# Performance work log

Measured on AMD Instinct MI355X. Metric: run time of the kernel, lower is better.

## Reference

```python
import jax, jax.numpy as jnp
import numpy as np

K = 1024
H = 16
HID = 4 * K
EPS = 1e-5


def _layernorm(x, g, b):
    mu = jnp.mean(x, axis=-1, keepdims=True)
    var = jnp.var(x, axis=-1, keepdims=True)
    return (x - mu) * jax.lax.rsqrt(var + EPS) * g + b


def _attention(xq, xkv, wq, wk, wv, wo, bo, causal):
    b, t, e = xq.shape
    tc = xkv.shape[1]
    h, s = H, e // H
    scale = e ** (-0.25)  # applied to both q and k, as in the original
    q = (xq @ wq).reshape(b, t, h, s) * scale
    k = (xkv @ wk).reshape(b, tc, h, s) * scale
    v = (xkv @ wv).reshape(b, tc, h, s)
    dot = jnp.einsum('bqhs,bkhs->bhqk', q, k)  # (b,h,t,tc)
    if causal:
        mask = jnp.tril(jnp.ones((t, tc), dtype=bool))
        dot = jnp.where(mask, dot, jnp.finfo(dot.dtype).min)
    att = jax.nn.softmax(dot, axis=-1)
    out = jnp.einsum('bhqk,bkhs->bqhs', att, v).reshape(b, t, e)
    return out @ wo + bo


def setup_inputs() -> dict:
    key = jax.random.key(0)
    ks = jax.random.split(key, 16)
    sd = K ** -0.5
    inp = {
        'x': jax.random.normal(ks[0], (4, 1024, K), jnp.float32),
        'context': jax.random.normal(ks[1], (4, 1024, K), jnp.float32),
        'sa_wq': jax.random.normal(ks[2], (K, K), jnp.float32) * sd,
        'sa_wk': jax.random.normal(ks[3], (K, K), jnp.float32) * sd,
        'sa_wv': jax.random.normal(ks[4], (K, K), jnp.float32) * sd,
        'sa_wo': jax.random.normal(ks[5], (K, K), jnp.float32) * sd,
        'sa_bo': jnp.zeros((K,), jnp.float32),
        'ca_wq': jax.random.normal(ks[6], (K, K), jnp.float32) * sd,
        'ca_wk': jax.random.normal(ks[7], (K, K), jnp.float32) * sd,
        'ca_wv': jax.random.normal(ks[8], (K, K), jnp.float32) * sd,
        'ca_wo': jax.random.normal(ks[9], (K, K), jnp.float32) * sd,
        'ca_bo': jnp.zeros((K,), jnp.float32),
        'n1_g': jnp.ones((K,), jnp.float32), 'n1_b': jnp.zeros((K,), jnp.float32),
        'n2_g': jnp.ones((K,), jnp.float32), 'n2_b': jnp.zeros((K,), jnp.float32),
        'n3_g': jnp.ones((K,), jnp.float32), 'n3_b': jnp.zeros((K,), jnp.float32),
        'ff_w1': jax.random.normal(ks[10], (K, HID), jnp.float32) * sd,
        'ff_b1': jnp.zeros((HID,), jnp.float32),
        'ff_w2': jax.random.normal(ks[11], (HID, K), jnp.float32) * (HID ** -0.5),
        'ff_b2': jnp.zeros((K,), jnp.float32),
    }
    return inp


def reference(x, context, sa_wq, sa_wk, sa_wv, sa_wo, sa_bo,
              ca_wq, ca_wk, ca_wv, ca_wo, ca_bo,
              n1_g, n1_b, n2_g, n2_b, n3_g, n3_b,
              ff_w1, ff_b1, ff_w2, ff_b2):
    # Masked self-attention + residual + LN (dropout is identity in eval mode)
    sa = _attention(x, x, sa_wq, sa_wk, sa_wv, sa_wo, sa_bo, causal=True)
    x = _layernorm(x + sa, n1_g, n1_b)
    # Cross-attention + residual + LN
    ca = _attention(x, context, ca_wq, ca_wk, ca_wv, ca_wo, ca_bo, causal=False)
    x = _layernorm(x + ca, n2_g, n2_b)
    # FFN + residual + LN
    ff = jax.nn.relu(x @ ff_w1 + ff_b1) @ ff_w2 + ff_b2
    x = _layernorm(x + ff, n3_g, n3_b)
    return x
```

## Files before the change

kernel.cpp:

```cpp
#include <hip/hip_runtime.h>

typedef __bf16 bf16x8 __attribute__((ext_vector_type(8)));
typedef __bf16 bf16x4 __attribute__((ext_vector_type(4)));
typedef float floatx4 __attribute__((ext_vector_type(4)));

#define EMB 1024
#define MROWS 4096
#define HIDN 4096
#define PSTRIDE ((size_t)MROWS * EMB)

__device__ __forceinline__ void load_lds16(const __bf16* g, __bf16* l) {
    __builtin_amdgcn_global_load_lds(
        (const __attribute__((address_space(1))) void*)g,
        (__attribute__((address_space(3))) void*)l, 16, 0, 0);
}

struct TJobs { const float* s[16]; __bf16* d[16]; int sld[16]; int dld[16]; };
__global__ void transpose_cast16_kernel(TJobs a) {
    __shared__ float tile[32][33];
    int jz = blockIdx.z;
    const float* in = a.s[jz];
    __bf16* out = a.d[jz];
    int sld = a.sld[jz], dld = a.dld[jz];
    int tx = threadIdx.x, ty = threadIdx.y;
    int c0 = blockIdx.x * 32, r0 = blockIdx.y * 32;
#pragma unroll
    for (int i = 0; i < 32; i += 8)
        tile[ty + i][tx] = in[(size_t)(r0 + ty + i) * sld + c0 + tx];
    __syncthreads();
#pragma unroll
    for (int i = 0; i < 32; i += 8)
        out[(size_t)(c0 + ty + i) * dld + r0 + tx] = (__bf16)tile[tx][ty + i];
}

__global__ void transpose_v_kernel(const __bf16* __restrict__ in,
                                   __bf16* __restrict__ vt, int ld, int Tc) {
    __shared__ __bf16 tile[32][33];
    int tx = threadIdx.x, ty = threadIdx.y;
    int t0 = blockIdx.x * 32, s0 = blockIdx.y * 32;
    int bh = blockIdx.z, b = bh >> 4, h = bh & 15;
#pragma unroll
    for (int i = 0; i < 32; i += 8)
        tile[ty + i][tx] = in[(size_t)(b * Tc + t0 + ty + i) * ld + h * 64 + s0 + tx];
    __syncthreads();
#pragma unroll
    for (int i = 0; i < 32; i += 8)
        vt[((size_t)bh * 64 + s0 + ty + i) * Tc + t0 + tx] = tile[tx][ty + i];
}

__global__ void cast_bf16_kernel(const float* __restrict__ in,
                                 __bf16* __restrict__ out, int n) {
    int i = (blockIdx.x * 256 + threadIdx.x) * 4;
    if (i >= n) return;
    float4 v = *(const float4*)(in + i);
    bf16x4 o;
    o[0] = (__bf16)v.x; o[1] = (__bf16)v.y; o[2] = (__bf16)v.z; o[3] = (__bf16)v.w;
    *(bf16x4*)(out + i) = o;
}

template <int RELU, int REG>
__launch_bounds__(256, 4)
__global__ void gemm_bt(const __bf16* __restrict__ A, const __bf16* __restrict__ A2,
                        int asplit, const __bf16* __restrict__ Bt,
                        __bf16* __restrict__ cb, __bf16* __restrict__ cbalt,
                        const float* __restrict__ bias,
                        int M, int N, int Kd, float scale0, float scale1,
                        int split, int fx, int fy) {
    __shared__ alignas(16) __bf16 smem[2 * 128 * 32];
    __bf16* As = smem;
    __bf16* Bs = smem + 128 * 32;
    int tid  = threadIdx.x;
    int wv   = tid >> 6, lane = tid & 63;

    int L   = blockIdx.x + gridDim.x * (blockIdx.y + gridDim.y * blockIdx.z);
    int xcd = L & 7, j = L >> 3;
    int ff  = fx * fy;
    int zw  = xcd / ff;
    int rr  = xcd % ff;
    int nxf = gridDim.x / fx;
    int bnw = (j % nxf) * fx + (rr % fx);
    int bmw = (j / nxf) * fy + (rr / fx);
    int bn  = bnw * 128, bm = bmw * 128;

    int wm   = (wv & 1) * 64, wn = (wv >> 1) * 64;
    int l16  = lane & 15, g16 = lane >> 4;

    int kc   = Kd / gridDim.z;
    int zoff = zw * kc;

    const __bf16* Ause = (bn >= asplit) ? A2 : A;

    const __bf16* ag0 = Ause + (size_t)(bm + (tid >> 2)) * Kd + zoff + (tid & 3) * 8;
    const __bf16* ag1 = ag0 + (size_t)64 * Kd;
    const __bf16* bg0 = Bt + (size_t)(bn + (tid >> 2)) * Kd + zoff + (tid & 3) * 8;
    const __bf16* bg1 = bg0 + (size_t)64 * Kd;
    __bf16* al0 = &As[tid * 8];
    __bf16* al1 = &As[2048 + tid * 8];
    __bf16* bl0 = &Bs[tid * 8];
    __bf16* bl1 = &Bs[2048 + tid * 8];

    floatx4 acc[4][4] = {};

    if (REG) {
        bf16x8 pa0 = *(const bf16x8*)ag0;
        bf16x8 pa1 = *(const bf16x8*)ag1;
        bf16x8 pb0 = *(const bf16x8*)bg0;
        bf16x8 pb1 = *(const bf16x8*)bg1;
        for (int k0 = 0; k0 < kc; k0 += 32) {
            *(bf16x8*)al0 = pa0;
            *(bf16x8*)al1 = pa1;
            *(bf16x8*)bl0 = pb0;
            *(bf16x8*)bl1 = pb1;
            if (k0 + 32 < kc) {
                ag0 += 32; ag1 += 32; bg0 += 32; bg1 += 32;
                pa0 = *(const bf16x8*)ag0;
                pa1 = *(const bf16x8*)ag1;
                pb0 = *(const bf16x8*)bg0;
                pb1 = *(const bf16x8*)bg1;
            }
            __syncthreads();
            bf16x8 af[4], bfr[4];
#pragma unroll
            for (int i = 0; i < 4; ++i)
                af[i] = *(const bf16x8*)&As[(wm + i * 16 + l16) * 32 + g16 * 8];
#pragma unroll
            for (int jj = 0; jj < 4; ++jj)
                bfr[jj] = *(const bf16x8*)&Bs[(wn + jj * 16 + l16) * 32 + g16 * 8];
#pragma unroll
            for (int i = 0; i < 4; ++i)
#pragma unroll
                for (int jj = 0; jj < 4; ++jj)
                    acc[i][jj] = __builtin_amdgcn_mfma_f32_16x16x32_bf16(af[i], bfr[jj], acc[i][jj], 0, 0, 0);
            __syncthreads();
        }
    } else {
        for (int k0 = 0; k0 < kc; k0 += 32) {
            __syncthreads();
            load_lds16(ag0, al0); load_lds16(ag1, al1);
            load_lds16(bg0, bl0); load_lds16(bg1, bl1);
            ag0 += 32; ag1 += 32; bg0 += 32; bg1 += 32;
            __syncthreads();
            bf16x8 af[4], bfr[4];
#pragma unroll
            for (int i = 0; i < 4; ++i)
                af[i] = *(const bf16x8*)&As[(wm + i * 16 + l16) * 32 + g16 * 8];
#pragma unroll
            for (int jj = 0; jj < 4; ++jj)
                bfr[jj] = *(const bf16x8*)&Bs[(wn + jj * 16 + l16) * 32 + g16 * 8];
#pragma unroll
            for (int i = 0; i < 4; ++i)
#pragma unroll
                for (int jj = 0; jj < 4; ++jj)
                    acc[i][jj] = __builtin_amdgcn_mfma_f32_16x16x32_bf16(af[i], bfr[jj], acc[i][jj], 0, 0, 0);
        }
        __syncthreads();
    }

    __bf16* Cp = (zw == 0) ? cb : cbalt + (size_t)(zw - 1) * M * N;
    const float* bz = (zw == 0) ? bias : nullptr;

    __bf16* eb = smem + wv * 2048;
    int erow = lane >> 2;
    int ecol = (lane & 3) * 16;
#pragma unroll
    for (int i = 0; i < 4; ++i) {
#pragma unroll
        for (int jj = 0; jj < 4; ++jj) {
            int col  = bn + wn + jj * 16 + l16;
            float sc = (col < split) ? scale0 : scale1;
            float bv = bz ? bz[col] : 0.f;
#pragma unroll
            for (int r = 0; r < 4; ++r) {
                float v = acc[i][jj][r] * sc + bv;
                if (RELU) v = fmaxf(v, 0.f);
                eb[(g16 * 4 + r) * 76 + jj * 16 + l16] = (__bf16)v;
            }
        }
        bf16x8 t0 = *(const bf16x8*)&eb[erow * 76 + ecol];
        bf16x8 t1 = *(const bf16x8*)&eb[erow * 76 + ecol + 8];
        size_t gb = (size_t)(bm + wm + i * 16 + erow) * N + bn + wn + ecol;
        *(bf16x8*)&Cp[gb]     = t0;
        *(bf16x8*)&Cp[gb + 8] = t1;
    }
}

__launch_bounds__(256, 3)
__global__ void attn_kernel(const __bf16* __restrict__ qb, const __bf16* __restrict__ kb,
                            const __bf16* __restrict__ vt, int ldq, int ldk,
                            __bf16* __restrict__ out, int causal, int Tc) {
    constexpr int T = 1024;
    __shared__ alignas(16) __bf16 Qs[128 * 72];
    __shared__ alignas(16) __bf16 Ks[64 * 72];
    __shared__ alignas(16) __bf16 Vs[64 * 72];
    __shared__ alignas(16) __bf16 Ps[4][16 * 72];

    int tid = threadIdx.x;
    int wv = tid >> 6, lane = tid & 63;
    int l16 = lane & 15, g16 = lane >> 4;

    int L = blockIdx.x;
    int xcd = L & 7, idx = L >> 3;
    int i3 = idx & 7;
    int qt2 = (idx & 32) ? (7 - i3) : i3;
    int pair = xcd + 8 * (idx >> 3);
    int h = pair & 15, b = pair >> 4;

    int r0 = tid >> 3, s8 = (tid & 7) * 8;
    int r1 = r0 + 32;

#pragma unroll
    for (int p = 0; p < 4; ++p) {
        int row = r0 + p * 32;
        bf16x8 qv = *(const bf16x8*)(qb + (size_t)(b * T + qt2 * 128 + row) * ldq + h * 64 + s8);
        *(bf16x8*)&Qs[row * 72 + s8] = qv;
    }

    floatx4 oacc[2][4] = {};
    float li[2] = {0.f, 0.f};

    int ktend = causal ? (2 * qt2 + 2) : (Tc / 64);

    const __bf16* kbase = kb + (size_t)b * Tc * ldk + h * 64 + s8;
    const __bf16* vbase = vt + (size_t)(b * 16 + h) * 64 * Tc + s8;

    bf16x8 kc0 = *(const bf16x8*)(kbase + (size_t)r0 * ldk);
    bf16x8 kc1 = *(const bf16x8*)(kbase + (size_t)r1 * ldk);
    bf16x8 vc0 = *(const bf16x8*)(vbase + (size_t)r0 * Tc);
    bf16x8 vc1 = *(const bf16x8*)(vbase + (size_t)r1 * Tc);
    bf16x8 kn0, kn1, vn0, vn1;

    for (int kt = 0; kt < ktend; ++kt) {
        __syncthreads();
        *(bf16x8*)&Ks[r0 * 72 + s8] = kc0;
        *(bf16x8*)&Ks[r1 * 72 + s8] = kc1;
        *(bf16x8*)&Vs[r0 * 72 + s8] = vc0;
        *(bf16x8*)&Vs[r1 * 72 + s8] = vc1;
        if (kt + 1 < ktend) {
            const __bf16* kp = kbase + (size_t)(kt + 1) * 64 * ldk;
            const __bf16* vp = vbase + (size_t)(kt + 1) * 64;
            kn0 = *(const bf16x8*)(kp + (size_t)r0 * ldk);
            kn1 = *(const bf16x8*)(kp + (size_t)r1 * ldk);
            vn0 = *(const bf16x8*)(vp + (size_t)r0 * Tc);
            vn1 = *(const bf16x8*)(vp + (size_t)r1 * Tc);
        }
        __syncthreads();

#pragma unroll
        for (int sub = 0; sub < 2; ++sub) {
            if (causal && kt > 2 * qt2 + sub) continue;

            floatx4 sacc[4] = {};
#pragma unroll
            for (int kk = 0; kk < 2; ++kk) {
                bf16x8 bq = *(const bf16x8*)&Qs[(sub * 64 + wv * 16 + l16) * 72 + kk * 32 + g16 * 8];
#pragma unroll
                for (int j = 0; j < 4; ++j) {
                    bf16x8 ak = *(const bf16x8*)&Ks[(j * 16 + l16) * 72 + kk * 32 + g16 * 8];
                    sacc[j] = __builtin_amdgcn_mfma_f32_16x16x32_bf16(ak, bq, sacc[j], 0, 0, 0);
                }
            }
            if (causal && kt == 2 * qt2 + sub) {
                int qloc = wv * 16 + l16;
#pragma unroll
                for (int j = 0; j < 4; ++j)
#pragma unroll
                    for (int r = 0; r < 4; ++r)
                        if (j * 16 + g16 * 4 + r > qloc) sacc[j][r] = -1e30f;
            }

#pragma unroll
            for (int j = 0; j < 4; ++j) {
                bf16x4 pk;
#pragma unroll
                for (int r = 0; r < 4; ++r) {
                    float p = __builtin_amdgcn_exp2f(sacc[j][r]);
                    li[sub] += p;
                    pk[r] = (__bf16)p;
                }
                *(bf16x4*)&Ps[wv][l16 * 72 + j * 16 + g16 * 4] = pk;
            }
#pragma unroll
            for (int kk = 0; kk < 2; ++kk) {
                bf16x8 bp = *(const bf16x8*)&Ps[wv][l16 * 72 + kk * 32 + g16 * 8];
#pragma unroll
                for (int j = 0; j < 4; ++j) {
                    bf16x8 av = *(const bf16x8*)&Vs[(j * 16 + l16) * 72 + kk * 32 + g16 * 8];
                    oacc[sub][j] = __builtin_amdgcn_mfma_f32_16x16x32_bf16(av, bp, oacc[sub][j], 0, 0, 0);
                }
            }
        }
        kc0 = kn0; kc1 = kn1; vc0 = vn0; vc1 = vn1;
    }

    li[0] += __shfl_xor(li[0], 16); li[0] += __shfl_xor(li[0], 32);
    li[1] += __shfl_xor(li[1], 16); li[1] += __shfl_xor(li[1], 32);

    __syncthreads();
    int rw = lane >> 2, c4 = (lane & 3) * 16;
#pragma unroll
    for (int sub = 0; sub < 2; ++sub) {
        float inv = 1.f / li[sub];
#pragma unroll
        for (int j = 0; j < 4; ++j) {
            bf16x4 ok;
#pragma unroll
            for (int r = 0; r < 4; ++r) ok[r] = (__bf16)(oacc[sub][j][r] * inv);
            *(bf16x4*)&Ks[(wv * 16 + l16) * 72 + j * 16 + g16 * 4] = ok;
        }
        bf16x8 o0 = *(const bf16x8*)&Ks[(wv * 16 + rw) * 72 + c4];
        bf16x8 o1 = *(const bf16x8*)&Ks[(wv * 16 + rw) * 72 + c4 + 8];
        size_t ob = (size_t)(b * T + qt2 * 128 + sub * 64 + wv * 16 + rw) * EMB + h * 64 + c4;
        *(bf16x8*)&out[ob]     = o0;
        *(bf16x8*)&out[ob + 8] = o1;
    }
}

__launch_bounds__(256)
__global__ void ln_kernel(const float* __restrict__ res,
                          const __bf16* __restrict__ pb, int np,
                          const float* __restrict__ g, const float* __restrict__ be,
                          float* __restrict__ outf, __bf16* __restrict__ outb) {
    __shared__ float red[8];
    int row = blockIdx.x, tid = threadIdx.x;
    size_t base = (size_t)row * EMB;
    float4 v = ((const float4*)(res + base))[tid];
    for (int i = 0; i < np; ++i) {
        bf16x4 u = *(const bf16x4*)(pb + i * PSTRIDE + base + tid * 4);
        v.x += (float)u[0]; v.y += (float)u[1];
        v.z += (float)u[2]; v.w += (float)u[3];
    }
    float s  = v.x + v.y + v.z + v.w;
    float ss = v.x * v.x + v.y * v.y + v.z * v.z + v.w * v.w;
#pragma unroll
    for (int o = 1; o < 64; o <<= 1) { s += __shfl_xor(s, o); ss += __shfl_xor(ss, o); }
    if ((tid & 63) == 0) { red[(tid >> 6) * 2] = s; red[(tid >> 6) * 2 + 1] = ss; }
    __syncthreads();
    s  = red[0] + red[2] + red[4] + red[6];
    ss = red[1] + red[3] + red[5] + red[7];
    float mu  = s * (1.0f / 1024.0f);
    float var = ss * (1.0f / 1024.0f) - mu * mu;
    float rs  = rsqrtf(var + 1e-5f);
    float4 gg = ((const float4*)g)[tid];
    float4 bb = ((const float4*)be)[tid];
    float4 y;
    y.x = (v.x - mu) * rs * gg.x + bb.x;
    y.y = (v.y - mu) * rs * gg.y + bb.y;
    y.z = (v.z - mu) * rs * gg.z + bb.z;
    y.w = (v.w - mu) * rs * gg.w + bb.w;
    ((float4*)(outf + base))[tid] = y;
    if (outb) {
        bf16x4 o;
        o[0] = (__bf16)y.x; o[1] = (__bf16)y.y; o[2] = (__bf16)y.z; o[3] = (__bf16)y.w;
        *(bf16x4*)(outb + base + tid * 4) = o;
    }
}

extern "C" void kernel_launch(void* const* d_in, const int* in_sizes, int n_in,
                              void* d_out, int out_size, void* d_ws, size_t ws_size,
                              hipStream_t stream) {
    const float* x     = (const float*)d_in[0];
    const float* ctx   = (const float*)d_in[1];
    const float* sa_wq = (const float*)d_in[2];
    const float* sa_wk = (const float*)d_in[3];
    const float* sa_wv = (const float*)d_in[4];
    const float* sa_wo = (const float*)d_in[5];
    const float* sa_bo = (const float*)d_in[6];
    const float* ca_wq = (const float*)d_in[7];
    const float* ca_wk = (const float*)d_in[8];
    const float* ca_wv = (const float*)d_in[9];
    const float* ca_wo = (const float*)d_in[10];
    const float* ca_bo = (const float*)d_in[11];
    const float* n1_g = (const float*)d_in[12];
    const float* n1_b = (const float*)d_in[13];
    const float* n2_g = (const float*)d_in[14];
    const float* n2_b = (const float*)d_in[15];
    const float* n3_g = (const float*)d_in[16];
    const float* n3_b = (const float*)d_in[17];
    const float* ff_w1 = (const float*)d_in[18];
    const float* ff_b1 = (const float*)d_in[19];
    const float* ff_w2 = (const float*)d_in[20];
    const float* ff_b2 = (const float*)d_in[21];

    size_t off = 0;
    auto alloc = [&](size_t bytes) {
        void* p = (char*)d_ws + off;
        off += (bytes + 255) & ~(size_t)255;
        return p;
    };
    __bf16* w_sa_qkvT = (__bf16*)alloc((size_t)3 * EMB * EMB * 2);
    __bf16* w_sa_oT   = (__bf16*)alloc((size_t)EMB * EMB * 2);
    __bf16* w_ca_kvqT = (__bf16*)alloc((size_t)3 * EMB * EMB * 2);
    __bf16* w_ca_oT   = (__bf16*)alloc((size_t)EMB * EMB * 2);
    __bf16* w1T       = (__bf16*)alloc((size_t)HIDN * EMB * 2);
    __bf16* w2T       = (__bf16*)alloc((size_t)EMB * HIDN * 2);
    __bf16* xb        = (__bf16*)alloc((size_t)MROWS * EMB * 2);
    __bf16* qkv       = (__bf16*)alloc((size_t)MROWS * 3 * EMB * 2);
    __bf16* ao        = (__bf16*)alloc((size_t)MROWS * EMB * 2);
    __bf16* hid       = (__bf16*)alloc((size_t)MROWS * HIDN * 2);
    __bf16* x1b       = (__bf16*)alloc((size_t)MROWS * EMB * 2);
    __bf16* vt        = (__bf16*)alloc((size_t)MROWS * EMB * 2);
    float* res1       = (float*)alloc((size_t)MROWS * EMB * 4);
    float* res2       = (float*)alloc((size_t)MROWS * EMB * 4);

    __bf16* qkvc = qkv;
    __bf16* pbo  = qkv;
    __bf16* pbf  = xb;

    const float QSC = 0.04508422002778011f;
    const int   BIG = 1 << 30;
    dim3 tb(32, 8);

    TJobs tj;
    tj.s[0] = sa_wq; tj.d[0] = w_sa_qkvT;                          tj.sld[0] = EMB;  tj.dld[0] = EMB;
    tj.s[1] = sa_wk; tj.d[1] = w_sa_qkvT + (size_t)EMB * EMB;      tj.sld[1] = EMB;  tj.dld[1] = EMB;
    tj.s[2] = sa_wv; tj.d[2] = w_sa_qkvT + (size_t)2 * EMB * EMB;  tj.sld[2] = EMB;  tj.dld[2] = EMB;
    tj.s[3] = sa_wo; tj.d[3] = w_sa_oT;                            tj.sld[3] = EMB;  tj.dld[3] = EMB;
    tj.s[4] = ca_wk; tj.d[4] = w_ca_kvqT;                          tj.sld[4] = EMB;  tj.dld[4] = EMB;
    tj.s[5] = ca_wv; tj.d[5] = w_ca_kvqT + (size_t)EMB * EMB;      tj.sld[5] = EMB;  tj.dld[5] = EMB;
    tj.s[6] = ca_wq; tj.d[6] = w_ca_kvqT + (size_t)2 * EMB * EMB;  tj.sld[6] = EMB;  tj.dld[6] = EMB;
    tj.s[7] = ca_wo; tj.d[7] = w_ca_oT;                            tj.sld[7] = EMB;  tj.dld[7] = EMB;
    for (int c = 0; c < 4; ++c) {
        tj.s[8 + c] = ff_w1 + (size_t)c * 1024;
        tj.d[8 + c] = w1T + (size_t)c * 1024 * 1024;
        tj.sld[8 + c] = HIDN; tj.dld[8 + c] = EMB;
    }
    for (int c = 0; c < 4; ++c) {
        tj.s[12 + c] = ff_w2 + (size_t)c * 1024 * 1024;
        tj.d[12 + c] = w2T + (size_t)c * 1024;
        tj.sld[12 + c] = EMB; tj.dld[12 + c] = HIDN;
    }
    transpose_cast16_kernel<<<dim3(32, 32, 16), tb, 0, stream>>>(tj);

    cast_bf16_kernel<<<4096, 256, 0, stream>>>(x, xb, MROWS * EMB);
    gemm_bt<0, 0><<<dim3(24, 32), 256, 0, stream>>>(xb, xb, BIG, w_sa_qkvT,
        qkv, nullptr, nullptr, MROWS, 3 * EMB, EMB, QSC, 1.f, 1024, 2, 4);
    transpose_v_kernel<<<dim3(32, 2, 64), tb, 0, stream>>>(qkv + 2 * EMB, vt, 3 * EMB, 1024);
    attn_kernel<<<512, 256, 0, stream>>>(qkv, qkv + EMB, vt, 3 * EMB, 3 * EMB, ao, 1, 1024);
    gemm_bt<0, 1><<<dim3(8, 32, 2), 256, 0, stream>>>(ao, ao, BIG, w_sa_oT,
        pbo, pbo + PSTRIDE, sa_bo, MROWS, EMB, EMB, 1.f, 1.f, 0, 2, 2);
    ln_kernel<<<4096, 256, 0, stream>>>(x, pbo, 2, n1_g, n1_b, res1, x1b);

    cast_bf16_kernel<<<4096, 256, 0, stream>>>(ctx, xb, MROWS * EMB);
    gemm_bt<0, 0><<<dim3(24, 32), 256, 0, stream>>>(xb, x1b, 2048, w_ca_kvqT,
        qkvc, nullptr, nullptr, MROWS, 3 * EMB, EMB, 1.f, QSC, 2048, 2, 4);
    transpose_v_kernel<<<dim3(32, 2, 64), tb, 0, stream>>>(qkvc + EMB, vt, 3 * EMB, 1024);
    attn_kernel<<<512, 256, 0, stream>>>(qkvc + 2 * EMB, qkvc, vt, 3 * EMB, 3 * EMB, ao, 0, 1024);
    gemm_bt<0, 1><<<dim3(8, 32, 2), 256, 0, stream>>>(ao, ao, BIG, w_ca_oT,
        pbo, pbo + PSTRIDE, ca_bo, MROWS, EMB, EMB, 1.f, 1.f, 0, 2, 2);
    ln_kernel<<<4096, 256, 0, stream>>>(res1, pbo, 2, n2_g, n2_b, res2, x1b);

    gemm_bt<1, 0><<<dim3(32, 32), 256, 0, stream>>>(x1b, x1b, BIG, w1T,
        hid, nullptr, ff_b1, MROWS, HIDN, EMB, 1.f, 1.f, 0, 2, 4);
    gemm_bt<0, 1><<<dim3(8, 32, 4), 256, 0, stream>>>(hid, hid, BIG, w2T,
        pbf, pbf + PSTRIDE, ff_b2, MROWS, EMB, HIDN, 1.f, 1.f, 0, 1, 2);
    ln_kernel<<<4096, 256, 0, stream>>>(res2, pbf, 4, n3_g, n3_b, (float*)d_out, nullptr);
}
```

Measured before the change: 460.5 us.

## Add 256x256-tile pipelined GEMM for QKV and FFN1 projections

Introduces a new 512-thread GEMM kernel with 256x256 output tiles, double-buffered LDS filled by direct global-to-LDS loads, and XOR-swizzled LDS addressing. The main loop is split into eight phases that interleave loads for the next tile with MFMA work, using explicit vmcnt waits, barriers and setprio. Block indices are mapped with an XCD-aware remap. It replaces the older gemm for the two QKV projections and the first FFN matmul, aiming for more data reuse per block and better overlap of memory and compute. The cost is more register and LDS pressure and fewer blocks per launch, which could cause tail or occupancy problems.

```diff
diff --git a/kernel.cpp b/kernel.cpp
--- a/kernel.cpp
+++ b/kernel.cpp
@@ -181,6 +181,152 @@
         size_t gb = (size_t)(bm + wm + i * 16 + erow) * N + bn + wn + ecol;
         *(bf16x8*)&Cp[gb]     = t0;
         *(bf16x8*)&Cp[gb + 8] = t1;
+    }
+}
+
+
+#define VM4 asm volatile("s_waitcnt vmcnt(4)" ::: "memory")
+#define VM0 asm volatile("s_waitcnt vmcnt(0)" ::: "memory")
+
+#define STG(GB, HROWS, LDST, TILE)                                             \
+    do {                                                                       \
+        load_lds16((GB) + (size_t)(HROWS) * Kd + (TILE) * 64, (LDST) + tid8);  \
+        load_lds16((GB) + (size_t)((HROWS) + 128) * Kd + (TILE) * 64,          \
+                   (LDST) + 4096 + tid8);                                      \
+    } while (0)
+
+#define PHASE(ABUF, BBUF, QM, QN, STAGE, TAIL)                                  \
+    {                                                                           \
+        bf16x8 a_[4][2], b_[2][2];                                              \
+        _Pragma("unroll")                                                       \
+        for (int i2 = 0; i2 < 4; ++i2) {                                        \
+            int s_ = (QM) * 128 + wr64 + i2 * 16 + l16;                         \
+            a_[i2][0] = *(const bf16x8*)&(ABUF)[s_ * 64 + pa0];                 \
+            a_[i2][1] = *(const bf16x8*)&(ABUF)[s_ * 64 + pa1];                 \
+        }                                                                       \
+        _Pragma("unroll")                                                       \
+        for (int j2 = 0; j2 < 2; ++j2) {                                        \
+            int s_ = (QN) * 128 + wc32 + j2 * 16 + l16;                         \
+            b_[j2][0] = *(const bf16x8*)&(BBUF)[s_ * 64 + pa0];                 \
+            b_[j2][1] = *(const bf16x8*)&(BBUF)[s_ * 64 + pa1];                 \
+        }                                                                       \
+        STAGE;                                                                  \
+        __builtin_amdgcn_s_barrier();                                           \
+        asm volatile("s_waitcnt lgkmcnt(0)" ::: "memory");                      \
+        __builtin_amdgcn_s_setprio(1);                                          \
+        _Pragma("unroll")                                                       \
+        for (int i2 = 0; i2 < 4; ++i2)                                          \
+            _Pragma("unroll")                                                   \
+            for (int j2 = 0; j2 < 2; ++j2) {                                    \
+                acc[(QM) * 4 + i2][(QN) * 2 + j2] =                             \
+                    __builtin_amdgcn_mfma_f32_16x16x32_bf16(                    \
+                        a_[i2][0], b_[j2][0],                                   \
+                        acc[(QM) * 4 + i2][(QN) * 2 + j2], 0, 0, 0);            \
+                acc[(QM) * 4 + i2][(QN) * 2 + j2] =                             \
+                    __builtin_amdgcn_mfma_f32_16x16x32_bf16(                    \
+                        a_[i2][1], b_[j2][1],                                   \
+                        acc[(QM) * 4 + i2][(QN) * 2 + j2], 0, 0, 0);            \
+            }                                                                   \
+        __builtin_amdgcn_s_setprio(0);                                          \
+        TAIL;                                                                   \
+        __builtin_amdgcn_s_barrier();                                           \
+    }
+
+template <int RELU>
+__launch_bounds__(512, 2)
+__global__ void gemm256(const __bf16* __restrict__ A, const __bf16* __restrict__ A2,
+                        int asplit, const __bf16* __restrict__ Bt,
+                        __bf16* __restrict__ C, const float* __restrict__ bias,
+                        int N, int Kd, float scale0, float scale1,
+                        int split, int pw) {
+    __shared__ alignas(16) __bf16 smem[65536];
+    __bf16* Alds0 = smem;
+    __bf16* Alds1 = smem + 16384;
+    __bf16* Blds0 = smem + 32768;
+    __bf16* Blds1 = smem + 49152;
+
+    int tid = threadIdx.x;
+    int wv = tid >> 6, lane = tid & 63;
+    int l16 = lane & 15, g16 = lane >> 4;
+    int wr = wv >> 2, wc = wv & 3;
+    int wr64 = wr * 64, wc32 = wc * 32;
+    int pa0 = (g16 ^ (l16 & 7)) * 8;
+    int pa1 = pa0 ^ 32;
+
+    int L = blockIdx.x;
+    int xcd = L & 7, jj = L >> 3;
+    int bm = ((xcd >> 1) * 4 + jj / pw) * 256;
+    int bn = ((xcd & 1) * pw + jj % pw) * 256;
+
+    const __bf16* Ause = (bn >= asplit) ? A2 : A;
+    int tid8 = tid * 8;
+    int colOff = ((tid & 7) ^ ((tid >> 3) & 7)) * 8;
+    const __bf16* baseA = Ause + (size_t)(bm + (tid >> 3)) * Kd + colOff;
+    const __bf16* baseB = Bt + (size_t)(bn + (tid >> 8) * 64 + ((tid >> 3) & 31)) * Kd + colOff;
+
+    floatx4 acc[8][4] = {};
+
+    STG(baseA, 0,  Alds0,        0);
+    STG(baseB, 0,  Blds0,        0);
+    STG(baseA, 64, Alds0 + 8192, 0);
+    STG(baseB, 32, Blds0 + 8192, 0);
+    STG(baseA, 0,  Alds1,        1);
+    STG(baseB, 0,  Blds1,        1);
+    VM4;
+    __builtin_amdgcn_s_barrier();
+
+    int niter = Kd >> 7;
+    for (int t = 0; t < niter - 1; ++t) {
+        int tv = 2 * t + 1, tn0 = 2 * t + 2, tn1 = 2 * t + 3;
+        PHASE(Alds0, Blds0, 0, 0, STG(baseA, 64, Alds1 + 8192, tv),  (void)0);
+        PHASE(Alds0, Blds0, 0, 1, STG(baseB, 32, Blds1 + 8192, tv),  (void)0);
+        PHASE(Alds0, Blds0, 1, 0, STG(baseA, 0,  Alds0,        tn0), (void)0);
+        PHASE(Alds0, Blds0, 1, 1, STG(baseB, 0,  Blds0,        tn0), VM4);
+        PHASE(Alds1, Blds1, 0, 0, STG(baseA, 64, Alds0 + 8192, tn0), (void)0);
+        PHASE(Alds1, Blds1, 0, 1, STG(baseB, 32, Blds0 + 8192, tn0), (void)0);
+        PHASE(Alds1, Blds1, 1, 0, STG(baseA, 0,  Alds1,        tn1), (void)0);
+        PHASE(Alds1, Blds1, 1, 1, STG(baseB, 0,  Blds1,        tn1), VM4);
+    }
+    {
+        int tv = (Kd >> 6) - 1;
+        PHASE(Alds0, Blds0, 0, 0, STG(baseA, 64, Alds1 + 8192, tv), (void)0);
+        PHASE(Alds0, Blds0, 0, 1, STG(baseB, 32, Blds1 + 8192, tv), (void)0);
+        PHASE(Alds0, Blds0, 1, 0, (void)0, (void)0);
+        PHASE(Alds0, Blds0, 1, 1, (void)0, VM0);
+        PHASE(Alds1, Blds1, 0, 0, (void)0, (void)0);
+        PHASE(Alds1, Blds1, 0, 1, (void)0, (void)0);
+        PHASE(Alds1, Blds1, 1, 0, (void)0, (void)0);
+        PHASE(Alds1, Blds1, 1, 1, (void)0, (void)0);
+    }
+
+    __syncthreads();
+
+    __bf16* eb = smem + wv * 1216;
+    int erow = lane >> 2;
+    int ecol = (lane & 3) * 16;
+    float sc[4], bv[4];
+#pragma unroll
+    for (int j = 0; j < 4; ++j) {
+        int col = bn + wc * 64 + j * 16 + l16;
+        sc[j] = (col < split) ? scale0 : scale1;
+        bv[j] = bias ? bias[col] : 0.f;
+    }
+#pragma unroll
+    for (int i = 0; i < 8; ++i) {
+#pragma unroll
+        for (int j = 0; j < 4; ++j) {
+#pragma unroll
+            for (int r = 0; r < 4; ++r) {
+                float v = acc[i][j][r] * sc[j] + bv[j];
+                if (RELU) v = fmaxf(v, 0.f);
+                eb[(g16 * 4 + r) * 76 + j * 16 + l16] = (__bf16)v;
+            }
+        }
+        bf16x8 t0 = *(const bf16x8*)&eb[erow * 76 + ecol];
+        bf16x8 t1 = *(const bf16x8*)&eb[erow * 76 + ecol + 8];
+        size_t gb = (size_t)(bm + wr * 128 + i * 16 + erow) * N + bn + wc * 64 + ecol;
+        *(bf16x8*)&C[gb]     = t0;
+        *(bf16x8*)&C[gb + 8] = t1;
     }
 }
 
@@ -432,8 +578,8 @@
     transpose_cast16_kernel<<<dim3(32, 32, 16), tb, 0, stream>>>(tj);
 
     cast_bf16_kernel<<<4096, 256, 0, stream>>>(x, xb, MROWS * EMB);
-    gemm_bt<0, 0><<<dim3(24, 32), 256, 0, stream>>>(xb, xb, BIG, w_sa_qkvT,
-        qkv, nullptr, nullptr, MROWS, 3 * EMB, EMB, QSC, 1.f, 1024, 2, 4);
+    gemm256<0><<<192, 512, 0, stream>>>(xb, xb, BIG, w_sa_qkvT,
+        qkv, nullptr, 3 * EMB, EMB, QSC, 1.f, 1024, 6);
     transpose_v_kernel<<<dim3(32, 2, 64), tb, 0, stream>>>(qkv + 2 * EMB, vt, 3 * EMB, 1024);
     attn_kernel<<<512, 256, 0, stream>>>(qkv, qkv + EMB, vt, 3 * EMB, 3 * EMB, ao, 1, 1024);
     gemm_bt<0, 1><<<dim3(8, 32, 2), 256, 0, stream>>>(ao, ao, BIG, w_sa_oT,
@@ -441,16 +587,16 @@
     ln_kernel<<<4096, 256, 0, stream>>>(x, pbo, 2, n1_g, n1_b, res1, x1b);
 
     cast_bf16_kernel<<<4096, 256, 0, stream>>>(ctx, xb, MROWS * EMB);
-    gemm_bt<0, 0><<<dim3(24, 32), 256, 0, stream>>>(xb, x1b, 2048, w_ca_kvqT,
-        qkvc, nullptr, nullptr, MROWS, 3 * EMB, EMB, 1.f, QSC, 2048, 2, 4);
+    gemm256<0><<<192, 512, 0, stream>>>(xb, x1b, 2048, w_ca_kvqT,
+        qkvc, nullptr, 3 * EMB, EMB, 1.f, QSC, 2048, 6);
     transpose_v_kernel<<<dim3(32, 2, 64), tb, 0, stream>>>(qkvc + EMB, vt, 3 * EMB, 1024);
     attn_kernel<<<512, 256, 0, stream>>>(qkvc + 2 * EMB, qkvc, vt, 3 * EMB, 3 * EMB, ao, 0, 1024);
     gemm_bt<0, 1><<<dim3(8, 32, 2), 256, 0, stream>>>(ao, ao, BIG, w_ca_oT,
         pbo, pbo + PSTRIDE, ca_bo, MROWS, EMB, EMB, 1.f, 1.f, 0, 2, 2);
     ln_kernel<<<4096, 256, 0, stream>>>(res1, pbo, 2, n2_g, n2_b, res2, x1b);
 
-    gemm_bt<1, 0><<<dim3(32, 32), 256, 0, stream>>>(x1b, x1b, BIG, w1T,
-        hid, nullptr, ff_b1, MROWS, HIDN, EMB, 1.f, 1.f, 0, 2, 4);
+    gemm256<1><<<256, 512, 0, stream>>>(x1b, x1b, BIG, w1T,
+        hid, ff_b1, HIDN, EMB, 1.f, 1.f, 0, 8);
     gemm_bt<0, 1><<<dim3(8, 32, 4), 256, 0, stream>>>(hid, hid, BIG, w2T,
         pbf, pbf + PSTRIDE, ff_b2, MROWS, EMB, HIDN, 1.f, 1.f, 0, 1, 2);
     ln_kernel<<<4096, 256, 0, stream>>>(res2, pbf, 4, n3_g, n3_b, (float*)d_out, nullptr);
```

Measured after the change: 461.7 us. About the same (+0.3%).
